# Optimization experiments

Hardware: AMD Instinct MI355X
Metric: run time of the kernel (lower is better)

The kernel has to match this reference:

```python
import jax, jax.numpy as jnp
import numpy as np

N_TREES, DEPTH, INPUT_DIM, N_CLASSES = 15, 3, 128, 10
N_LEAVES = 2 ** DEPTH
N_INTERNAL = N_LEAVES - 1


def _path_masks(depth):
    """Right/left ancestor indicator matrices [n_leaves, n_internal]."""
    n_leaves = 2 ** depth
    n_int = n_leaves - 1
    R = np.zeros((n_leaves, n_int), np.float32)
    L = np.zeros((n_leaves, n_int), np.float32)
    for leaf in range(n_leaves):
        node = leaf + n_int
        for _ in range(depth):
            parent = (node - 1) // 2
            if node % 2 == 0:
                R[leaf, parent] = 1.0
            else:
                L[leaf, parent] = 1.0
            node = parent
    return R, L

_R, _L = _path_masks(DEPTH)


def setup_inputs() -> dict:
    key = jax.random.key(0)
    k1, k2 = jax.random.split(key)
    batch = 262144
    per_tree = N_INTERNAL * INPUT_DIM + N_INTERNAL + N_LEAVES * N_CLASSES
    total = N_TREES * per_tree + N_TREES
    x = jax.random.normal(k1, (batch, INPUT_DIM), dtype=jnp.float32)
    params = jax.random.normal(k2, (total,), dtype=jnp.float32)
    return {"x": x, "params": params}


def reference(x, params):
    per_tree = N_INTERNAL * INPUT_DIM + N_INTERNAL + N_LEAVES * N_CLASSES
    blocks = params[: N_TREES * per_tree].reshape(N_TREES, per_tree)
    w_end = N_INTERNAL * INPUT_DIM
    split_w = blocks[:, :w_end].reshape(N_TREES, N_INTERNAL, INPUT_DIM)
    split_b = blocks[:, w_end : w_end + N_INTERNAL]  # [T, n_internal]
    leaf_logits = blocks[:, w_end + N_INTERNAL :].reshape(N_TREES, N_LEAVES, N_CLASSES)
    tree_w_logits = params[N_TREES * per_tree :]  # [T]

    # split logits z: [B, T, n_internal]
    z = jnp.einsum("bd,tnd->btn", x, split_w) + split_b[None, :, :]
    log_p = jax.nn.log_sigmoid(z)        # log sigma(z)
    log_1mp = jax.nn.log_sigmoid(-z)     # log (1 - sigma(z))

    R = jnp.asarray(_R)
    L = jnp.asarray(_L)
    # path product in log domain: [B, T, n_leaves]
    leaf_probs = jnp.exp(
        jnp.einsum("btn,ln->btl", log_p, R) + jnp.einsum("btn,ln->btl", log_1mp, L)
    )

    leaf_class_probs = jax.nn.softmax(leaf_logits, axis=-1)  # [T, n_leaves, C]
    tree_pred = jnp.einsum("btl,tlc->btc", leaf_probs, leaf_class_probs)
    tree_weights = jax.nn.softmax(tree_w_logits, axis=0)     # [T]
    final_pred = jnp.einsum("btc,t->bc", tree_pred, tree_weights)
    return final_pred
```

## Files before the change

kernel.cpp:

```cpp
#include <hip/hip_runtime.h>
#include <hip/hip_fp16.h>


typedef float    f32x4 __attribute__((ext_vector_type(4)));
typedef _Float16 half8 __attribute__((ext_vector_type(8)));

#define TREES      15
#define IDIM       128
#define NCLS       10
#define NINT       7
#define NLVS       8
#define PER_TREE   (NINT*IDIM + NINT + NLVS*NCLS)
#define NODES      (TREES*NINT)
#define NPAD       112
#define KPAD       128
#define RSTR       272
#define NBLK       512

__global__ __launch_bounds__(256) void prep_kernel(const float* __restrict__ p,
                                                   _Float16* __restrict__ wq,
                                                   float* __restrict__ bq,
                                                   _Float16* __restrict__ wbT) {
    const int gid  = blockIdx.x * 256 + threadIdx.x;
    const int nthr = gridDim.x * 256;

    for (int i = gid; i < NPAD * IDIM; i += nthr) {
        int g = i >> 7, k = i & 127;
        float v = 0.f;
        if (g < NODES) {
            int t = g / NINT, n = g % NINT;
            v = p[t * PER_TREE + n * IDIM + k];
        }
        wq[i] = (_Float16)v;
    }
    for (int i = gid; i < NPAD; i += nthr) {
        float v = 0.f;
        if (i < NODES) {
            int t = i / NINT, n = i % NINT;
            v = p[t * PER_TREE + NINT * IDIM + n];
        }
        bq[i] = v;
    }
    const float* tl = p + TREES * PER_TREE;
    for (int i = gid; i < 16 * KPAD; i += nthr) {
        int c = i >> 7, k = i & 127;
        float v = 0.f;
        if (c < NCLS && k < TREES * NLVS) {
            int t = k >> 3, l = k & 7;
            const float* ll = p + t * PER_TREE + NINT * IDIM + NINT + l * NCLS;
            float mx = ll[0];
            #pragma unroll
            for (int j = 1; j < NCLS; ++j) mx = fmaxf(mx, ll[j]);
            float se = 0.f;
            #pragma unroll
            for (int j = 0; j < NCLS; ++j) se += __expf(ll[j] - mx);
            float lsm = __expf(ll[c] - mx) / se;

            float m2 = tl[0];
            #pragma unroll
            for (int j = 1; j < TREES; ++j) m2 = fmaxf(m2, tl[j]);
            float s2 = 0.f;
            #pragma unroll
            for (int j = 0; j < TREES; ++j) s2 += __expf(tl[j] - m2);
            float tw = __expf(tl[t] - m2) / s2;
            v = lsm * tw;
        }
        wbT[i] = (_Float16)v;
    }
}

__device__ __forceinline__ void dma_quarter(const float* __restrict__ x,
                                            long grow0, char* qdst, int lane) {
    const int slot = lane & 31;
    #pragma unroll
    for (int it = 0; it < 8; ++it) {
        int r   = 2 * it + (lane >> 5);
        int c16 = (slot - r) & 31;
        const float* gp = x + (grow0 + r) * IDIM + c16 * 4;
        __builtin_amdgcn_global_load_lds(
            (const __attribute__((address_space(1))) void*)gp,
            (__attribute__((address_space(3))) void*)(qdst + it * 1024),
            16, 0, 0);
    }
}

__global__ __launch_bounds__(256, 2) void tree_main(const float* __restrict__ x,
                                                    const _Float16* __restrict__ wq,
                                                    const float* __restrict__ bq,
                                                    const _Float16* __restrict__ wbT,
                                                    float* __restrict__ out,
                                                    int tpb) {
    __shared__ __align__(16) char lds[2][32768];

    const int tid  = threadIdx.x;
    const int lane = tid & 63;
    const int w    = tid >> 6;
    const int lm   = lane & 15;
    const int lq   = lane >> 4;
    const int rg   = lane >> 2;
    const int g    = lane & 3;

    const long tile0 = (long)blockIdx.x * tpb;

    dma_quarter(x, tile0 * 64 + 16 * w, &lds[0][w * 8192], lane);

    half8 bf[7][4];
    float bb[7];
    #pragma unroll
    for (int nt = 0; nt < 7; ++nt) {
        bb[nt] = bq[16 * nt + lm];
        #pragma unroll
        for (int s = 0; s < 4; ++s)
            bf[nt][s] = *reinterpret_cast<const half8*>(wq + (16 * nt + lm) * IDIM + 32 * s + 8 * lq);
    }
    half8 wbf[4];
    #pragma unroll
    for (int s = 0; s < 4; ++s)
        wbf[s] = *reinterpret_cast<const half8*>(wbT + lm * KPAD + 32 * s + 8 * lq);

    for (int i = 0; i < tpb; ++i) {
        char* qcur = &lds[i & 1][w * 8192];
        const long grow = (tile0 + i) * 64;

        asm volatile("" ::: "memory");
        if (i == 0) __builtin_amdgcn_s_waitcnt(0x0F70);
        else        __builtin_amdgcn_s_waitcnt(0x0F74);
        asm volatile("" ::: "memory");

        half8 af[4];
        #pragma unroll
        for (int s = 0; s < 4; ++s) {
            int cc = 8 * s + 2 * lq;
            f32x4 f0 = *(const f32x4*)(qcur + lm * 512 + (((cc     + lm) & 31) << 4));
            f32x4 f1 = *(const f32x4*)(qcur + lm * 512 + (((cc + 1 + lm) & 31) << 4));
            half8 a;
            #pragma unroll
            for (int j = 0; j < 4; ++j) {
                a[j]     = (_Float16)f0[j];
                a[j + 4] = (_Float16)f1[j];
            }
            af[s] = a;
        }

        if (i + 1 < tpb)
            dma_quarter(x, (tile0 + i + 1) * 64 + 16 * w, &lds[(i + 1) & 1][w * 8192], lane);

        #pragma unroll
        for (int nt = 0; nt < 7; ++nt) {
            f32x4 acc = {bb[nt], bb[nt], bb[nt], bb[nt]};
            #pragma unroll
            for (int s = 0; s < 4; ++s)
                acc = __builtin_amdgcn_mfma_f32_16x16x32_f16(af[s], bf[nt][s], acc, 0, 0, 0);
            int node = 16 * nt + lm;
            int col  = node + ((node * 9363) >> 16);
            #pragma unroll
            for (int r = 0; r < 4; ++r) {
                float z  = acc[r];
                float sg = __builtin_amdgcn_rcpf(1.0f + __expf(-z));
                *(_Float16*)(qcur + (4 * lq + r) * RSTR + col * 2) = (_Float16)sg;
            }
        }

        {
            const char* rowp = qcur + rg * RSTR;
            half8 hv[4];
            #pragma unroll
            for (int tt = 0; tt < 4; ++tt)
                hv[tt] = *(const half8*)(rowp + 64 * g + 16 * tt);
            half8 lv[4];
            #pragma unroll
            for (int tt = 0; tt < 4; ++tt) {
                float s0 = (float)hv[tt][0], s1 = (float)hv[tt][1], s2v = (float)hv[tt][2];
                float s3 = (float)hv[tt][3], s4 = (float)hv[tt][4], s5 = (float)hv[tt][5];
                float s6 = (float)hv[tt][6];
                float u1 = 1.f - s0, u2 = s0;
                float q1 = u1 * s1, q0 = u1 - q1;
                float q3 = u2 * s2v, q2 = u2 - q3;
                float L1 = q0 * s3, L0 = q0 - L1;
                float L3 = q1 * s4, L2 = q1 - L3;
                float L5 = q2 * s5, L4 = q2 - L5;
                float L7 = q3 * s6, L6 = q3 - L7;
                float m = (4 * g + tt < TREES) ? 1.f : 0.f;
                half8 lv8;
                lv8[0] = (_Float16)(L0 * m); lv8[1] = (_Float16)(L1 * m);
                lv8[2] = (_Float16)(L2 * m); lv8[3] = (_Float16)(L3 * m);
                lv8[4] = (_Float16)(L4 * m); lv8[5] = (_Float16)(L5 * m);
                lv8[6] = (_Float16)(L6 * m); lv8[7] = (_Float16)(L7 * m);
                lv[tt] = lv8;
            }
            #pragma unroll
            for (int tt = 0; tt < 4; ++tt)
                *(half8*)(qcur + rg * RSTR + 64 * g + 16 * tt) = lv[tt];
        }

        {
            half8 af2[4];
            #pragma unroll
            for (int s = 0; s < 4; ++s)
                af2[s] = *(const half8*)(qcur + lm * RSTR + 64 * s + 16 * lq);
            f32x4 a2 = {0.f, 0.f, 0.f, 0.f};
            #pragma unroll
            for (int s = 0; s < 4; ++s)
                a2 = __builtin_amdgcn_mfma_f32_16x16x32_f16(af2[s], wbf[s], a2, 0, 0, 0);
            if (lm < NCLS) {
                #pragma unroll
                for (int r = 0; r < 4; ++r)
                    out[(grow + 16 * w + 4 * lq + r) * NCLS + lm] = a2[r];
            }
        }
    }
}

extern "C" void kernel_launch(void* const* d_in, const int* in_sizes, int n_in,
                              void* d_out, int out_size, void* d_ws, size_t ws_size,
                              hipStream_t stream) {
    const float* x      = (const float*)d_in[0];
    const float* params = (const float*)d_in[1];
    float* out = (float*)d_out;

    _Float16* wq  = (_Float16*)d_ws;
    float*    bq  = (float*)((char*)d_ws + NPAD * IDIM * 2);
    _Float16* wbT = (_Float16*)((char*)bq + NPAD * 4);

    const int batch = in_sizes[0] / IDIM;
    const int tiles = batch / 64;
    const int tpb   = tiles / NBLK;

    prep_kernel<<<8, 256, 0, stream>>>(params, wq, bq, wbT);
    tree_main<<<NBLK, 256, 0, stream>>>(x, wq, bq, wbT, out, tpb);
}
```

Before: 203.1 us.

## Load x tiles directly into registers with double-buffered prefetch instead of LDS DMA

Replaces the global_load_lds DMA of x into a double-buffered LDS staging area with direct per-lane vector loads into two register sets that alternate across an unrolled-by-two tile loop. LDS shrinks to a small per-wave scratch used only for sigmoid and leaf-probability exchange. This removes the LDS round trip and explicit waitcnt for the input tile, but raises VGPR pressure and depends on the compiler to overlap the register loads. The loop also assumes an even tile count per block.

```diff
diff --git a/kernel.cpp b/kernel.cpp
--- a/kernel.cpp
+++ b/kernel.cpp
@@ -15,6 +15,7 @@
 #define NPAD       112
 #define KPAD       128
 #define RSTR       272
+#define WSTR       4352
 #define NBLK       512
 
 __global__ __launch_bounds__(256) void prep_kernel(const float* __restrict__ p,
@@ -69,18 +70,12 @@
     }
 }
 
-__device__ __forceinline__ void dma_quarter(const float* __restrict__ x,
-                                            long grow0, char* qdst, int lane) {
-    const int slot = lane & 31;
+__device__ __forceinline__ void load_xa(const float* __restrict__ xr,
+                                        f32x4 (&xa)[8]) {
     #pragma unroll
-    for (int it = 0; it < 8; ++it) {
-        int r   = 2 * it + (lane >> 5);
-        int c16 = (slot - r) & 31;
-        const float* gp = x + (grow0 + r) * IDIM + c16 * 4;
-        __builtin_amdgcn_global_load_lds(
-            (const __attribute__((address_space(1))) void*)gp,
-            (__attribute__((address_space(3))) void*)(qdst + it * 1024),
-            16, 0, 0);
+    for (int s = 0; s < 4; ++s) {
+        xa[2 * s]     = *(const f32x4*)(xr + 32 * s);
+        xa[2 * s + 1] = *(const f32x4*)(xr + 32 * s + 4);
     }
 }
 
@@ -90,7 +85,7 @@
                                                     const _Float16* __restrict__ wbT,
                                                     float* __restrict__ out,
                                                     int tpb) {
-    __shared__ __align__(16) char lds[2][32768];
+    __shared__ __align__(16) char lds[4 * WSTR];
 
     const int tid  = threadIdx.x;
     const int lane = tid & 63;
@@ -100,9 +95,13 @@
     const int rg   = lane >> 2;
     const int g    = lane & 3;
 
+    char* sbuf = &lds[w * WSTR];
     const long tile0 = (long)blockIdx.x * tpb;
 
-    dma_quarter(x, tile0 * 64 + 16 * w, &lds[0][w * 8192], lane);
+    const float* xlane = x + (tile0 * 64 + 16 * w + lm) * IDIM + 8 * lq;
+
+    f32x4 xaA[8], xaB[8];
+    load_xa(xlane, xaA);
 
     half8 bf[7][4];
     float bb[7];
@@ -118,32 +117,23 @@
     for (int s = 0; s < 4; ++s)
         wbf[s] = *reinterpret_cast<const half8*>(wbT + lm * KPAD + 32 * s + 8 * lq);
 
-    for (int i = 0; i < tpb; ++i) {
-        char* qcur = &lds[i & 1][w * 8192];
+    auto tile_body = [&](int i, f32x4 (&xac)[8], f32x4 (&xan)[8]) {
         const long grow = (tile0 + i) * 64;
-
-        asm volatile("" ::: "memory");
-        if (i == 0) __builtin_amdgcn_s_waitcnt(0x0F70);
-        else        __builtin_amdgcn_s_waitcnt(0x0F74);
-        asm volatile("" ::: "memory");
 
         half8 af[4];
         #pragma unroll
         for (int s = 0; s < 4; ++s) {
-            int cc = 8 * s + 2 * lq;
-            f32x4 f0 = *(const f32x4*)(qcur + lm * 512 + (((cc     + lm) & 31) << 4));
-            f32x4 f1 = *(const f32x4*)(qcur + lm * 512 + (((cc + 1 + lm) & 31) << 4));
             half8 a;
             #pragma unroll
             for (int j = 0; j < 4; ++j) {
-                a[j]     = (_Float16)f0[j];
-                a[j + 4] = (_Float16)f1[j];
+                a[j]     = (_Float16)xac[2 * s][j];
+                a[j + 4] = (_Float16)xac[2 * s + 1][j];
             }
             af[s] = a;
         }
 
         if (i + 1 < tpb)
-            dma_quarter(x, (tile0 + i + 1) * 64 + 16 * w, &lds[(i + 1) & 1][w * 8192], lane);
+            load_xa(xlane + (long)(i + 1) * 64 * IDIM, xan);
 
         #pragma unroll
         for (int nt = 0; nt < 7; ++nt) {
@@ -157,12 +147,12 @@
             for (int r = 0; r < 4; ++r) {
                 float z  = acc[r];
                 float sg = __builtin_amdgcn_rcpf(1.0f + __expf(-z));
-                *(_Float16*)(qcur + (4 * lq + r) * RSTR + col * 2) = (_Float16)sg;
+                *(_Float16*)(sbuf + (4 * lq + r) * RSTR + col * 2) = (_Float16)sg;
             }
         }
 
         {
-            const char* rowp = qcur + rg * RSTR;
+            const char* rowp = sbuf + rg * RSTR;
             half8 hv[4];
             #pragma unroll
             for (int tt = 0; tt < 4; ++tt)
@@ -190,14 +180,14 @@
             }
             #pragma unroll
             for (int tt = 0; tt < 4; ++tt)
-                *(half8*)(qcur + rg * RSTR + 64 * g + 16 * tt) = lv[tt];
+                *(half8*)(sbuf + rg * RSTR + 64 * g + 16 * tt) = lv[tt];
         }
 
         {
             half8 af2[4];
             #pragma unroll
             for (int s = 0; s < 4; ++s)
-                af2[s] = *(const half8*)(qcur + lm * RSTR + 64 * s + 16 * lq);
+                af2[s] = *(const half8*)(sbuf + lm * RSTR + 64 * s + 16 * lq);
             f32x4 a2 = {0.f, 0.f, 0.f, 0.f};
             #pragma unroll
             for (int s = 0; s < 4; ++s)
@@ -208,6 +198,11 @@
                     out[(grow + 16 * w + 4 * lq + r) * NCLS + lm] = a2[r];
             }
         }
+    };
+
+    for (int i = 0; i < tpb; i += 2) {
+        tile_body(i,     xaA, xaB);
+        tile_body(i + 1, xaB, xaA);
     }
 }
 
```

Result: slower. 208.4 us (+2.6%).
